# Kernel optimization log

Hardware: AMD Instinct MI355X
Metric: run time of the kernel (lower is better)

The kernel has to match this reference:

```python
import jax, jax.numpy as jnp
import numpy as np

B, S, D = 4, 2048, 1024
H = 16
HD = D // H  # 64


def setup_inputs() -> dict:
    key = jax.random.key(0)
    ks = jax.random.split(key, 8)
    scale = 1.0 / np.sqrt(D)
    return {
        "hidden_states": jax.random.normal(ks[0], (B, S, D), dtype=jnp.float32),
        "attention_mask": jnp.ones((B, 1, 1, S), dtype=jnp.int32),
        "Wq": jax.random.normal(ks[1], (D, D), dtype=jnp.float32) * scale,
        "bq": jax.random.normal(ks[2], (D,), dtype=jnp.float32) * 0.02,
        "Wk": jax.random.normal(ks[3], (D, D), dtype=jnp.float32) * scale,
        "bk": jax.random.normal(ks[4], (D,), dtype=jnp.float32) * 0.02,
        "Wv": jax.random.normal(ks[5], (D, D), dtype=jnp.float32) * scale,
        "bv": jax.random.normal(ks[6], (D,), dtype=jnp.float32) * 0.02,
    }


def _split_heads(x):
    # [b, t, (h d)] -> [b, h, t, d]
    b, t, _ = x.shape
    return x.reshape(b, t, H, HD).transpose(0, 2, 1, 3)


def reference(hidden_states, attention_mask, Wq, bq, Wk, bk, Wv, bv):
    # Linear projections (torch Linear: x @ W.T + b)
    q = _split_heads(hidden_states @ Wq.T + bq)
    k = _split_heads(hidden_states @ Wk.T + bk)
    v = _split_heads(hidden_states @ Wv.T + bv)

    # scaled dot-product scores: [b, h, s, s]
    scores = jnp.einsum("bhqd,bhkd->bhqk", q, k) / np.sqrt(HD)

    s = scores.shape[-1]
    causal = jnp.tril(jnp.ones((s, s), dtype=bool))[None, None]
    neg_inf = jnp.float32(-jnp.inf)
    scores = jnp.where(causal, scores, neg_inf)
    # attention_mask is 0/1 keep mask: [b, 1, 1, s]
    scores = jnp.where(attention_mask == 0, neg_inf, scores)

    probs = jax.nn.softmax(scores, axis=-1)  # dropout p=0 (eval)
    ctx = jnp.einsum("bhqk,bhkd->bhqd", probs, v)
    # [b, h, t, d] -> [b, t, h*d]
    return ctx.transpose(0, 2, 1, 3).reshape(hidden_states.shape[0], s, D)
```

## Files before the change

### kernel.cpp

```cpp
#include <hip/hip_runtime.h>
#include <hip/hip_bf16.h>
#include <math.h>


#define B_ 4
#define S_ 2048
#define D_ 1024
#define H_ 16
#define HD_ 64
#define M_ (B_ * S_)

typedef unsigned short u16;
typedef unsigned int u32;
typedef __attribute__((ext_vector_type(4))) float f32x4;
typedef __attribute__((ext_vector_type(8))) short bf16x8;

__device__ __forceinline__ u16 f2bfu_rn(float x) {
    u32 u = __builtin_bit_cast(u32, x);
    return (u16)((u + 0x8000u) >> 16);
}

__device__ __forceinline__ void gl2lds16(const void* g, void* l) {
    __builtin_amdgcn_global_load_lds(
        (const __attribute__((address_space(1))) u32*)g,
        (__attribute__((address_space(3))) u32*)l, 16, 0, 0);
}

#define XN  8388608u
#define WN  1048576u
__global__ __launch_bounds__(256) void convert_bf16(
    const float* __restrict__ X,  const float* __restrict__ Wq,
    const float* __restrict__ Wk, const float* __restrict__ Wv,
    u16* __restrict__ Xb, u16* __restrict__ Wqb,
    u16* __restrict__ Wkb, u16* __restrict__ Wvb)
{
    size_t idx = ((size_t)blockIdx.x * 256 + threadIdx.x) * 8;
    const float* src; u16* dst; size_t off;
    if (idx < XN)                { src = X;  dst = Xb;  off = idx; }
    else if (idx < XN + WN)      { src = Wq; dst = Wqb; off = idx - XN; }
    else if (idx < XN + 2 * WN)  { src = Wk; dst = Wkb; off = idx - XN - WN; }
    else                         { src = Wv; dst = Wvb; off = idx - XN - 2 * WN; }
    float4 a = *(const float4*)(src + off);
    float4 b = *(const float4*)(src + off + 4);
    uint4 o;
    o.x = (u32)f2bfu_rn(a.x) | ((u32)f2bfu_rn(a.y) << 16);
    o.y = (u32)f2bfu_rn(a.z) | ((u32)f2bfu_rn(a.w) << 16);
    o.z = (u32)f2bfu_rn(b.x) | ((u32)f2bfu_rn(b.y) << 16);
    o.w = (u32)f2bfu_rn(b.z) | ((u32)f2bfu_rn(b.w) << 16);
    *(uint4*)(dst + off) = o;
}

#define QSCALE 0.18033688011112042f

__global__ __launch_bounds__(256) void qkv_mfma(
    const u16* __restrict__ Xb,
    const u16* __restrict__ Wqb, const u16* __restrict__ Wkb,
    const u16* __restrict__ Wvb,
    const float* __restrict__ bq, const float* __restrict__ bk,
    const float* __restrict__ bv,
    u16* __restrict__ Qb, u16* __restrict__ Kb, u16* __restrict__ Vtb)
{
    const int which = blockIdx.z;
    const u16* Asrc; const u16* Bsrc; const float* bias; u16* Out;
    int m0, n0;
    if (which == 0)      { Asrc = Xb;  Bsrc = Wqb; bias = bq; Out = Qb;
                           m0 = blockIdx.y * 128; n0 = blockIdx.x * 128; }
    else if (which == 1) { Asrc = Xb;  Bsrc = Wkb; bias = bk; Out = Kb;
                           m0 = blockIdx.y * 128; n0 = blockIdx.x * 128; }
    else                 { Asrc = Wvb; Bsrc = Xb;  bias = bv; Out = Vtb;
                           m0 = blockIdx.x * 128; n0 = blockIdx.y * 128; }

    __shared__ u16 As[128][64];
    __shared__ u16 Bs[128][64];

    const int t = threadIdx.x;
    const int wave = t >> 6, lane = t & 63;
    const int qd = lane >> 4, l15 = lane & 15;
    const int wm = wave >> 1, wn = wave & 1;

    const f32x4 zero = {0.f, 0.f, 0.f, 0.f};
    f32x4 acc[4][4];
#pragma unroll
    for (int i = 0; i < 4; ++i)
#pragma unroll
        for (int j = 0; j < 4; ++j) acc[i][j] = zero;

    for (int k0 = 0; k0 < D_; k0 += 64) {
        __syncthreads();
#pragma unroll
        for (int i = 0; i < 4; ++i) {
            int r0  = (wave * 4 + i) * 8;
            int row = r0 + (lane >> 3);
            int g   = (lane & 7) ^ (row & 7);
            gl2lds16(Asrc + (size_t)(m0 + row) * D_ + k0 + g * 8, &As[r0][0]);
            gl2lds16(Bsrc + (size_t)(n0 + row) * D_ + k0 + g * 8, &Bs[r0][0]);
        }
        __syncthreads();
#pragma unroll
        for (int ks = 0; ks < 2; ++ks) {
            bf16x8 af[4], bf[4];
#pragma unroll
            for (int mt = 0; mt < 4; ++mt) {
                int row = wm * 64 + mt * 16 + l15;
                int p = (ks * 4 + qd) ^ (row & 7);
                af[mt] = *(const bf16x8*)&As[row][p * 8];
            }
#pragma unroll
            for (int nt = 0; nt < 4; ++nt) {
                int row = wn * 64 + nt * 16 + l15;
                int p = (ks * 4 + qd) ^ (row & 7);
                bf[nt] = *(const bf16x8*)&Bs[row][p * 8];
            }
#pragma unroll
            for (int mt = 0; mt < 4; ++mt)
#pragma unroll
                for (int nt = 0; nt < 4; ++nt)
                    acc[mt][nt] = __builtin_amdgcn_mfma_f32_16x16x32_bf16(
                        af[mt], bf[nt], acc[mt][nt], 0, 0, 0);
        }
    }

    if (which < 2) {
#pragma unroll
        for (int nt = 0; nt < 4; ++nt) {
            int n = n0 + wn * 64 + nt * 16 + l15;
            float bv_ = bias[n];
            int h = n >> 6, hd = n & 63;
#pragma unroll
            for (int mt = 0; mt < 4; ++mt)
#pragma unroll
                for (int r = 0; r < 4; ++r) {
                    int m = m0 + wm * 64 + mt * 16 + qd * 4 + r;
                    int bb = m >> 11, s = m & 2047;
                    float v = acc[mt][nt][r] + bv_;
                    if (which == 0) v *= QSCALE;
                    Out[(((size_t)(bb * H_ + h)) * S_ + s) * HD_ + hd] = f2bfu_rn(v);
                }
        }
    } else {
#pragma unroll
        for (int mt = 0; mt < 4; ++mt)
#pragma unroll
            for (int r = 0; r < 4; ++r) {
                int f = m0 + wm * 64 + mt * 16 + qd * 4 + r;
                float bv_ = bias[f];
                int h = f >> 6, hd = f & 63;
#pragma unroll
                for (int nt = 0; nt < 4; ++nt) {
                    int tok = n0 + wn * 64 + nt * 16 + l15;
                    int bb = tok >> 11, s = tok & 2047;
                    float v = acc[mt][nt][r] + bv_;
                    Out[(((size_t)(bb * H_ + h)) * HD_ + hd) * S_ + s] = f2bfu_rn(v);
                }
            }
    }
}

__global__ __launch_bounds__(256) void attn_mfma(
    const u16* __restrict__ Qb, const u16* __restrict__ Kb,
    const u16* __restrict__ Vtb, const int* __restrict__ amask,
    float* __restrict__ Out)
{
    const int bh = blockIdx.y;
    const int b = bh >> 4, h = bh & 15;
    const int qt = (int)(gridDim.x - 1) - (int)blockIdx.x;
    const int q0 = qt * 64;
    const int t = threadIdx.x;
    const int wave = t >> 6, lane = t & 63;
    const int qd = lane >> 4, l15 = lane & 15;

    __shared__ u16 Ks[64][64];
    __shared__ u16 Vts[64][64];
    __shared__ u16 Ps[64][72];
    __shared__ float mb[64];

    const size_t base = (size_t)bh * S_ * HD_;
    const u16* Qg = Qb + base;
    const u16* Kg = Kb + base;
    const u16* Vg = Vtb + base;

    bf16x8 qf[2];
    {
        const u16* qrow = Qg + (size_t)(q0 + wave * 16 + l15) * HD_;
        qf[0] = *(const bf16x8*)(qrow + qd * 8);
        qf[1] = *(const bf16x8*)(qrow + 32 + qd * 8);
    }
    bf16x8 onesf;
    {
        short v = (l15 == 0) ? (short)0x3F80 : (short)0;
        onesf = (bf16x8){v, v, v, v, v, v, v, v};
    }

    const f32x4 zero = {0.f, 0.f, 0.f, 0.f};
    f32x4 o[5];
#pragma unroll
    for (int i = 0; i < 5; ++i) o[i] = zero;

    for (int jt = 0; jt <= qt; ++jt) {
        const int j0 = jt * 64;
        __syncthreads();
#pragma unroll
        for (int i = 0; i < 2; ++i) {
            int r0  = (wave * 2 + i) * 8;
            int row = r0 + (lane >> 3);
            int g   = (lane & 7) ^ (row & 7);
            gl2lds16(Kg + (size_t)(j0 + row) * HD_ + g * 8, &Ks[r0][0]);
            gl2lds16(Vg + (size_t)row * S_ + j0 + g * 8, &Vts[r0][0]);
        }
        if (t < 64) mb[t] = (amask[b * S_ + j0 + t] == 0) ? -1e30f : 0.0f;
        __syncthreads();

        f32x4 sacc[4];
#pragma unroll
        for (int nt = 0; nt < 4; ++nt) sacc[nt] = zero;
#pragma unroll
        for (int ks = 0; ks < 2; ++ks) {
#pragma unroll
            for (int nt = 0; nt < 4; ++nt) {
                int brow = nt * 16 + l15;
                int bp = (ks * 4 + qd) ^ (brow & 7);
                bf16x8 bf = *(const bf16x8*)&Ks[brow][bp * 8];
                sacc[nt] = __builtin_amdgcn_mfma_f32_16x16x32_bf16(
                    qf[ks], bf, sacc[nt], 0, 0, 0);
            }
        }

        float bias[4];
#pragma unroll
        for (int nt = 0; nt < 4; ++nt) bias[nt] = mb[nt * 16 + l15];
        const bool diag = (jt == qt);
#pragma unroll
        for (int r = 0; r < 4; ++r) {
            int prow = wave * 16 + qd * 4 + r;
#pragma unroll
            for (int nt = 0; nt < 4; ++nt) {
                int col = nt * 16 + l15;
                float s = sacc[nt][r] + bias[nt];
                if (diag && col > (prow)) s = -1e30f;
                float p = __builtin_amdgcn_exp2f(s);
                Ps[prow][col] = f2bfu_rn(p);
            }
        }

#pragma unroll
        for (int ks = 0; ks < 2; ++ks) {
            int arow = wave * 16 + l15;
            bf16x8 pf = *(const bf16x8*)&Ps[arow][ks * 32 + qd * 8];
#pragma unroll
            for (int nt = 0; nt < 4; ++nt) {
                int brow = nt * 16 + l15;
                int bp = (ks * 4 + qd) ^ (brow & 7);
                bf16x8 vf = *(const bf16x8*)&Vts[brow][bp * 8];
                o[nt] = __builtin_amdgcn_mfma_f32_16x16x32_bf16(
                    pf, vf, o[nt], 0, 0, 0);
            }
            o[4] = __builtin_amdgcn_mfma_f32_16x16x32_bf16(
                pf, onesf, o[4], 0, 0, 0);
        }
    }

#pragma unroll
    for (int r = 0; r < 4; ++r) {
        float l = __shfl(o[4][r], lane & 48);
        float inv = 1.0f / l;
        int q = q0 + wave * 16 + qd * 4 + r;
#pragma unroll
        for (int nt = 0; nt < 4; ++nt) {
            int hd = nt * 16 + l15;
            Out[((size_t)(b * S_ + q)) * D_ + h * HD_ + hd] = o[nt][r] * inv;
        }
    }
}

extern "C" void kernel_launch(void* const* d_in, const int* in_sizes, int n_in,
                              void* d_out, int out_size, void* d_ws, size_t ws_size,
                              hipStream_t stream) {
    (void)in_sizes; (void)n_in; (void)out_size; (void)ws_size;
    const float* X    = (const float*)d_in[0];
    const int*   mask = (const int*)d_in[1];
    const float* Wq   = (const float*)d_in[2];
    const float* bq   = (const float*)d_in[3];
    const float* Wk   = (const float*)d_in[4];
    const float* bk   = (const float*)d_in[5];
    const float* Wv   = (const float*)d_in[6];
    const float* bv   = (const float*)d_in[7];
    float* out = (float*)d_out;

    u16* Xb  = (u16*)d_ws;
    u16* Wqb = Xb  + XN;
    u16* Wkb = Wqb + WN;
    u16* Wvb = Wkb + WN;
    u16* Qb  = Wvb + WN;
    u16* Kb  = Qb  + XN;
    u16* Vtb = Kb  + XN;

    convert_bf16<<<(XN + 3 * WN) / (256 * 8), 256, 0, stream>>>(
        X, Wq, Wk, Wv, Xb, Wqb, Wkb, Wvb);
    qkv_mfma<<<dim3(D_ / 128, M_ / 128, 3), 256, 0, stream>>>(
        Xb, Wqb, Wkb, Wvb, bq, bk, bv, Qb, Kb, Vtb);
    attn_mfma<<<dim3(S_ / 64, B_ * H_), 256, 0, stream>>>(
        Qb, Kb, Vtb, mask, out);
}
```

Baseline: 281.8 us.

## Double query tile per block and double-buffer K/V loads in attention

Each attention block now covers 128 query rows: every wave handles two 16-row slabs, so each K/V tile staged in LDS is reused across twice as many queries. K/V tiles are double-buffered, with the next tile's global-to-LDS load issued before the current tile is computed, and there is one barrier per iteration. The mask bias is read directly from global memory per lane instead of being staged in LDS. This halves the grid and raises register and LDS use per block, which may reduce occupancy and worsen load balance across the causal triangle.

```diff
diff --git a/kernel.cpp b/kernel.cpp
--- a/kernel.cpp
+++ b/kernel.cpp
@@ -164,26 +164,27 @@
     const int bh = blockIdx.y;
     const int b = bh >> 4, h = bh & 15;
     const int qt = (int)(gridDim.x - 1) - (int)blockIdx.x;
-    const int q0 = qt * 64;
+    const int q0 = qt * 128;
     const int t = threadIdx.x;
     const int wave = t >> 6, lane = t & 63;
     const int qd = lane >> 4, l15 = lane & 15;
 
-    __shared__ u16 Ks[64][64];
-    __shared__ u16 Vts[64][64];
-    __shared__ u16 Ps[64][72];
-    __shared__ float mb[64];
+    __shared__ u16 Ks[2][64][64];
+    __shared__ u16 Vts[2][64][64];
+    __shared__ u16 Ps[128][72];
 
     const size_t base = (size_t)bh * S_ * HD_;
     const u16* Qg = Qb + base;
     const u16* Kg = Kb + base;
     const u16* Vg = Vtb + base;
-
-    bf16x8 qf[2];
-    {
-        const u16* qrow = Qg + (size_t)(q0 + wave * 16 + l15) * HD_;
-        qf[0] = *(const bf16x8*)(qrow + qd * 8);
-        qf[1] = *(const bf16x8*)(qrow + 32 + qd * 8);
+    const int* am = amask + b * S_;
+
+    bf16x8 qf[2][2];
+#pragma unroll
+    for (int s = 0; s < 2; ++s) {
+        const u16* qrow = Qg + (size_t)(q0 + (wave + 4 * s) * 16 + l15) * HD_;
+        qf[s][0] = *(const bf16x8*)(qrow + qd * 8);
+        qf[s][1] = *(const bf16x8*)(qrow + 32 + qd * 8);
     }
     bf16x8 onesf;
     {
@@ -192,84 +193,122 @@
     }
 
     const f32x4 zero = {0.f, 0.f, 0.f, 0.f};
-    f32x4 o[5];
-#pragma unroll
-    for (int i = 0; i < 5; ++i) o[i] = zero;
-
-    for (int jt = 0; jt <= qt; ++jt) {
+    f32x4 o[2][5];
+#pragma unroll
+    for (int s = 0; s < 2; ++s)
+#pragma unroll
+        for (int i = 0; i < 5; ++i) o[s][i] = zero;
+
+    const int nT = 2 * qt + 2;
+
+#pragma unroll
+    for (int i = 0; i < 2; ++i) {
+        int r0  = wave * 16 + i * 8;
+        int row = r0 + (lane >> 3);
+        int g   = (lane & 7) ^ (row & 7);
+        gl2lds16(Kg + (size_t)row * HD_ + g * 8, &Ks[0][r0][0]);
+        gl2lds16(Vg + (size_t)row * S_ + g * 8, &Vts[0][r0][0]);
+    }
+    __syncthreads();
+
+    for (int jt = 0; jt < nT; ++jt) {
         const int j0 = jt * 64;
-        __syncthreads();
-#pragma unroll
-        for (int i = 0; i < 2; ++i) {
-            int r0  = (wave * 2 + i) * 8;
-            int row = r0 + (lane >> 3);
-            int g   = (lane & 7) ^ (row & 7);
-            gl2lds16(Kg + (size_t)(j0 + row) * HD_ + g * 8, &Ks[r0][0]);
-            gl2lds16(Vg + (size_t)row * S_ + j0 + g * 8, &Vts[r0][0]);
-        }
-        if (t < 64) mb[t] = (amask[b * S_ + j0 + t] == 0) ? -1e30f : 0.0f;
-        __syncthreads();
-
-        f32x4 sacc[4];
-#pragma unroll
-        for (int nt = 0; nt < 4; ++nt) sacc[nt] = zero;
+        const int buf = jt & 1;
+
+        if (jt + 1 < nT) {
+            const int j1 = j0 + 64;
+#pragma unroll
+            for (int i = 0; i < 2; ++i) {
+                int r0  = wave * 16 + i * 8;
+                int row = r0 + (lane >> 3);
+                int g   = (lane & 7) ^ (row & 7);
+                gl2lds16(Kg + (size_t)(j1 + row) * HD_ + g * 8, &Ks[buf ^ 1][r0][0]);
+                gl2lds16(Vg + (size_t)row * S_ + j1 + g * 8, &Vts[buf ^ 1][r0][0]);
+            }
+        }
+
+        float kb[4];
+#pragma unroll
+        for (int nt = 0; nt < 4; ++nt)
+            kb[nt] = (am[j0 + nt * 16 + l15] == 0) ? -1e30f : 0.0f;
+
+        f32x4 sacc[2][4];
+#pragma unroll
+        for (int s = 0; s < 2; ++s)
+#pragma unroll
+            for (int nt = 0; nt < 4; ++nt) sacc[s][nt] = zero;
 #pragma unroll
         for (int ks = 0; ks < 2; ++ks) {
 #pragma unroll
             for (int nt = 0; nt < 4; ++nt) {
                 int brow = nt * 16 + l15;
                 int bp = (ks * 4 + qd) ^ (brow & 7);
-                bf16x8 bf = *(const bf16x8*)&Ks[brow][bp * 8];
-                sacc[nt] = __builtin_amdgcn_mfma_f32_16x16x32_bf16(
-                    qf[ks], bf, sacc[nt], 0, 0, 0);
-            }
-        }
-
-        float bias[4];
-#pragma unroll
-        for (int nt = 0; nt < 4; ++nt) bias[nt] = mb[nt * 16 + l15];
-        const bool diag = (jt == qt);
-#pragma unroll
-        for (int r = 0; r < 4; ++r) {
-            int prow = wave * 16 + qd * 4 + r;
-#pragma unroll
-            for (int nt = 0; nt < 4; ++nt) {
-                int col = nt * 16 + l15;
-                float s = sacc[nt][r] + bias[nt];
-                if (diag && col > (prow)) s = -1e30f;
-                float p = __builtin_amdgcn_exp2f(s);
-                Ps[prow][col] = f2bfu_rn(p);
+                bf16x8 kf = *(const bf16x8*)&Ks[buf][brow][bp * 8];
+                sacc[0][nt] = __builtin_amdgcn_mfma_f32_16x16x32_bf16(
+                    qf[0][ks], kf, sacc[0][nt], 0, 0, 0);
+                sacc[1][nt] = __builtin_amdgcn_mfma_f32_16x16x32_bf16(
+                    qf[1][ks], kf, sacc[1][nt], 0, 0, 0);
+            }
+        }
+
+#pragma unroll
+        for (int s = 0; s < 2; ++s) {
+            const int qbase = q0 + (wave + 4 * s) * 16;
+            const bool dg = (j0 + 63) > qbase;
+#pragma unroll
+            for (int r = 0; r < 4; ++r) {
+                int prow = (wave + 4 * s) * 16 + qd * 4 + r;
+                int q    = qbase + qd * 4 + r;
+#pragma unroll
+                for (int nt = 0; nt < 4; ++nt) {
+                    int col = nt * 16 + l15;
+                    float sv = sacc[s][nt][r] + kb[nt];
+                    if (dg && (j0 + col > q)) sv = -1e30f;
+                    float p = __builtin_amdgcn_exp2f(sv);
+                    Ps[prow][col] = f2bfu_rn(p);
+                }
             }
         }
 
 #pragma unroll
         for (int ks = 0; ks < 2; ++ks) {
-            int arow = wave * 16 + l15;
-            bf16x8 pf = *(const bf16x8*)&Ps[arow][ks * 32 + qd * 8];
+            bf16x8 pf[2];
+#pragma unroll
+            for (int s = 0; s < 2; ++s) {
+                int arow = (wave + 4 * s) * 16 + l15;
+                pf[s] = *(const bf16x8*)&Ps[arow][ks * 32 + qd * 8];
+            }
 #pragma unroll
             for (int nt = 0; nt < 4; ++nt) {
                 int brow = nt * 16 + l15;
                 int bp = (ks * 4 + qd) ^ (brow & 7);
-                bf16x8 vf = *(const bf16x8*)&Vts[brow][bp * 8];
-                o[nt] = __builtin_amdgcn_mfma_f32_16x16x32_bf16(
-                    pf, vf, o[nt], 0, 0, 0);
-            }
-            o[4] = __builtin_amdgcn_mfma_f32_16x16x32_bf16(
-                pf, onesf, o[4], 0, 0, 0);
-        }
-    }
-
-#pragma unroll
-    for (int r = 0; r < 4; ++r) {
-        float l = __shfl(o[4][r], lane & 48);
-        float inv = 1.0f / l;
-        int q = q0 + wave * 16 + qd * 4 + r;
-#pragma unroll
-        for (int nt = 0; nt < 4; ++nt) {
-            int hd = nt * 16 + l15;
-            Out[((size_t)(b * S_ + q)) * D_ + h * HD_ + hd] = o[nt][r] * inv;
-        }
-    }
+                bf16x8 vf = *(const bf16x8*)&Vts[buf][brow][bp * 8];
+                o[0][nt] = __builtin_amdgcn_mfma_f32_16x16x32_bf16(
+                    pf[0], vf, o[0][nt], 0, 0, 0);
+                o[1][nt] = __builtin_amdgcn_mfma_f32_16x16x32_bf16(
+                    pf[1], vf, o[1][nt], 0, 0, 0);
+            }
+            o[0][4] = __builtin_amdgcn_mfma_f32_16x16x32_bf16(
+                pf[0], onesf, o[0][4], 0, 0, 0);
+            o[1][4] = __builtin_amdgcn_mfma_f32_16x16x32_bf16(
+                pf[1], onesf, o[1][4], 0, 0, 0);
+        }
+
+        __syncthreads();
+    }
+
+#pragma unroll
+    for (int s = 0; s < 2; ++s)
+#pragma unroll
+        for (int r = 0; r < 4; ++r) {
+            float l = __shfl(o[s][4][r], lane & 48);
+            float inv = 1.0f / l;
+            int q = q0 + (wave + 4 * s) * 16 + qd * 4 + r;
+            float* op = Out + ((size_t)(b * S_ + q)) * D_ + h * HD_;
+#pragma unroll
+            for (int nt = 0; nt < 4; ++nt)
+                op[nt * 16 + l15] = o[s][nt][r] * inv;
+        }
 }
 
 extern "C" void kernel_launch(void* const* d_in, const int* in_sizes, int n_in,
@@ -298,6 +337,6 @@
         X, Wq, Wk, Wv, Xb, Wqb, Wkb, Wvb);
     qkv_mfma<<<dim3(D_ / 128, M_ / 128, 3), 256, 0, stream>>>(
         Xb, Wqb, Wkb, Wvb, bq, bk, bv, Qb, Kb, Vtb);
-    attn_mfma<<<dim3(S_ / 64, B_ * H_), 256, 0, stream>>>(
+    attn_mfma<<<dim3(S_ / 128, B_ * H_), 256, 0, stream>>>(
         Qb, Kb, Vtb, mask, out);
 }
```

New measurement: 302.0 us. +7.2%, slower.

## Split long causal attention rows across two blocks and combine partials

Applied to the files above, without the earlier changes.

Query tiles in the second half of the sequence now have their key range split into two chunks: keys 0-1023 and keys 1024 to the diagonal. Each chunk goes to its own block, and a new combine kernel sums the unnormalised outputs and row sums. This evens out per-block work for causal attention, where the last tiles used to take far longer than the others. In exchange it adds a kernel launch, extra workspace traffic for the partial outputs and sums, and a read-modify-write pass over half of the output.

```diff
diff --git a/kernel.cpp b/kernel.cpp
--- a/kernel.cpp
+++ b/kernel.cpp
@@ -156,15 +156,20 @@
     }
 }
 
-__global__ __launch_bounds__(256) void attn_mfma(
+__global__ __launch_bounds__(256) void attn_chunk(
     const u16* __restrict__ Qb, const u16* __restrict__ Kb,
     const u16* __restrict__ Vtb, const int* __restrict__ amask,
-    float* __restrict__ Out)
+    float* __restrict__ Oout, float* __restrict__ Opart,
+    float* __restrict__ L0, float* __restrict__ L1)
 {
+    const int x = blockIdx.x;
     const int bh = blockIdx.y;
     const int b = bh >> 4, h = bh & 15;
-    const int qt = (int)(gridDim.x - 1) - (int)blockIdx.x;
+    int qt, jt0, jt1; bool second;
+    if (x < 32) { qt = 31 - x; jt0 = 0;  jt1 = min(qt, 15); second = false; }
+    else        { qt = 63 - x; jt0 = 16; jt1 = qt;          second = true;  }
     const int q0 = qt * 64;
+
     const int t = threadIdx.x;
     const int wave = t >> 6, lane = t & 63;
     const int qd = lane >> 4, l15 = lane & 15;
@@ -178,6 +183,7 @@
     const u16* Qg = Qb + base;
     const u16* Kg = Kb + base;
     const u16* Vg = Vtb + base;
+    const int* am = amask + b * S_;
 
     bf16x8 qf[2];
     {
@@ -196,7 +202,7 @@
 #pragma unroll
     for (int i = 0; i < 5; ++i) o[i] = zero;
 
-    for (int jt = 0; jt <= qt; ++jt) {
+    for (int jt = jt0; jt <= jt1; ++jt) {
         const int j0 = jt * 64;
         __syncthreads();
 #pragma unroll
@@ -207,7 +213,7 @@
             gl2lds16(Kg + (size_t)(j0 + row) * HD_ + g * 8, &Ks[r0][0]);
             gl2lds16(Vg + (size_t)row * S_ + j0 + g * 8, &Vts[r0][0]);
         }
-        if (t < 64) mb[t] = (amask[b * S_ + j0 + t] == 0) ? -1e30f : 0.0f;
+        if (t < 64) mb[t] = (am[j0 + t] == 0) ? -1e30f : 0.0f;
         __syncthreads();
 
         f32x4 sacc[4];
@@ -236,7 +242,7 @@
             for (int nt = 0; nt < 4; ++nt) {
                 int col = nt * 16 + l15;
                 float s = sacc[nt][r] + bias[nt];
-                if (diag && col > (prow)) s = -1e30f;
+                if (diag && col > prow) s = -1e30f;
                 float p = __builtin_amdgcn_exp2f(s);
                 Ps[prow][col] = f2bfu_rn(p);
             }
@@ -259,17 +265,63 @@
         }
     }
 
-#pragma unroll
-    for (int r = 0; r < 4; ++r) {
-        float l = __shfl(o[4][r], lane & 48);
-        float inv = 1.0f / l;
-        int q = q0 + wave * 16 + qd * 4 + r;
-#pragma unroll
-        for (int nt = 0; nt < 4; ++nt) {
-            int hd = nt * 16 + l15;
-            Out[((size_t)(b * S_ + q)) * D_ + h * HD_ + hd] = o[nt][r] * inv;
-        }
-    }
+    if (!second) {
+        if (qt <= 15) {
+#pragma unroll
+            for (int r = 0; r < 4; ++r) {
+                float l = __shfl(o[4][r], lane & 48);
+                float inv = 1.0f / l;
+                int q = q0 + wave * 16 + qd * 4 + r;
+                float* op = Oout + ((size_t)(b * S_ + q)) * D_ + h * HD_;
+#pragma unroll
+                for (int nt = 0; nt < 4; ++nt)
+                    op[nt * 16 + l15] = o[nt][r] * inv;
+            }
+        } else {
+#pragma unroll
+            for (int r = 0; r < 4; ++r) {
+                int q = q0 + wave * 16 + qd * 4 + r;
+                float* op = Oout + ((size_t)(b * S_ + q)) * D_ + h * HD_;
+#pragma unroll
+                for (int nt = 0; nt < 4; ++nt)
+                    op[nt * 16 + l15] = o[nt][r];
+                if (l15 == 0) L0[(size_t)bh * S_ + q] = o[4][r];
+            }
+        }
+    } else {
+#pragma unroll
+        for (int r = 0; r < 4; ++r) {
+            int q = q0 + wave * 16 + qd * 4 + r;
+            int sh = q - 1024;
+            float* op = Opart + ((size_t)bh * 1024 + sh) * HD_;
+#pragma unroll
+            for (int nt = 0; nt < 4; ++nt)
+                op[nt * 16 + l15] = o[nt][r];
+            if (l15 == 0) L1[(size_t)bh * 1024 + sh] = o[4][r];
+        }
+    }
+}
+
+__global__ __launch_bounds__(256) void combine(
+    float* __restrict__ out, const float* __restrict__ Opart,
+    const float* __restrict__ L0, const float* __restrict__ L1)
+{
+    size_t i = ((size_t)blockIdx.x * 256 + threadIdx.x) * 4;
+    int d  = (int)(i & (D_ - 1));
+    int bs = (int)(i >> 10);
+    int b  = bs >> 10, sh = bs & 1023;
+    int s  = sh + 1024;
+    int h  = d >> 6;
+    int bh = b * H_ + h;
+    float l = L0[(size_t)bh * S_ + s] + L1[(size_t)bh * 1024 + sh];
+    float inv = 1.0f / l;
+    float* op = out + ((size_t)(b * S_ + s)) * D_ + d;
+    const float* pp = Opart + ((size_t)bh * 1024 + sh) * HD_ + (d & 63);
+    float4 v = *(float4*)op;
+    float4 p = *(const float4*)pp;
+    v.x = (v.x + p.x) * inv; v.y = (v.y + p.y) * inv;
+    v.z = (v.z + p.z) * inv; v.w = (v.w + p.w) * inv;
+    *(float4*)op = v;
 }
 
 extern "C" void kernel_launch(void* const* d_in, const int* in_sizes, int n_in,
@@ -293,11 +345,15 @@
     u16* Qb  = Wvb + WN;
     u16* Kb  = Qb  + XN;
     u16* Vtb = Kb  + XN;
+    float* Opart = (float*)(Vtb + XN);
+    float* L0 = Opart + (size_t)64 * 1024 * 64;
+    float* L1 = L0 + (size_t)64 * 2048;
 
     convert_bf16<<<(XN + 3 * WN) / (256 * 8), 256, 0, stream>>>(
         X, Wq, Wk, Wv, Xb, Wqb, Wkb, Wvb);
     qkv_mfma<<<dim3(D_ / 128, M_ / 128, 3), 256, 0, stream>>>(
         Xb, Wqb, Wkb, Wvb, bq, bk, bv, Qb, Kb, Vtb);
-    attn_mfma<<<dim3(S_ / 64, B_ * H_), 256, 0, stream>>>(
-        Qb, Kb, Vtb, mask, out);
-}
+    attn_chunk<<<dim3(48, B_ * H_), 256, 0, stream>>>(
+        Qb, Kb, Vtb, mask, out, Opart, L0, L1);
+    combine<<<(B_ * 1024 * D_ / 4) / 256, 256, 0, stream>>>(out, Opart, L0, L1);
+}
```

Result: faster. 265.1 us (-5.9%).
